# Optimization experiments

Hardware: AMD Instinct MI355X
Metric: run time of the kernel (lower is better)

Reference implementation:

```python
import jax, jax.numpy as jnp
import numpy as np

B, N, D, H, R, K = 64, 197, 768, 3072, 16, 1


def setup_inputs() -> dict:
    key = jax.random.key(0)
    ks = jax.random.split(key, 9)
    s1 = 1.0 / np.sqrt(D)
    s2 = 1.0 / np.sqrt(H)
    return {
        "x": jax.random.normal(ks[0], (B, N, D), dtype=jnp.float32),
        "W1": jax.random.normal(ks[1], (H, D), dtype=jnp.float32) * s1,
        "b1": jax.random.normal(ks[2], (H,), dtype=jnp.float32) * s1,
        "A1": jax.random.normal(ks[3], (K, R, D), dtype=jnp.float32) * s1,
        "B1": jax.random.normal(ks[4], (K, H, R), dtype=jnp.float32) * 0.01,
        "W2": jax.random.normal(ks[5], (D, H), dtype=jnp.float32) * s2,
        "b2": jax.random.normal(ks[6], (D,), dtype=jnp.float32) * s2,
        "A2": jax.random.normal(ks[7], (K, R, H), dtype=jnp.float32) * s2,
        "B2": jax.random.normal(ks[8], (K, D, R), dtype=jnp.float32) * 0.01,
    }


def _lora(x, A, Bm):
    # result of torch: (B @ (A @ x^T.unsqueeze(1))).sum(1).transpose(1,2)
    # A: [K, r, d_in], Bm: [K, d_out, r], x: [b, n, d_in] -> [b, n, d_out]
    t = jnp.einsum('krd,bnd->bknr', A, x)          # low-rank projection
    return jnp.einsum('kor,bknr->bno', Bm, t)      # expand + sum over K


def reference(x, W1, b1, A1, B1, W2, b2, A2, B2):
    # fc1 (Linear + LoRA correction)
    h = jnp.einsum('bnd,hd->bnh', x, W1) + b1 + _lora(x, A1, B1)
    # exact (erf-based) GELU, matching torch nn.GELU default
    h = jax.nn.gelu(h, approximate=False)
    # dropout p=0 and norm=Identity by default -> no-ops
    out = jnp.einsum('bnh,dh->bnd', h, W2) + b2 + _lora(h, A2, B2)
    return out
```

## Files before the change

### kernel.cpp

```cpp
#include <hip/hip_runtime.h>
#include <math.h>

#define M_ROWS 12608
#define D_DIM  768
#define H_DIM  3072

typedef __bf16 bf16_t;
typedef __bf16 bf16x8 __attribute__((ext_vector_type(8)));
typedef float  f32x4  __attribute__((ext_vector_type(4)));

__device__ __forceinline__ void gl2lds16(const bf16_t* g, bf16_t* l) {
  __builtin_amdgcn_global_load_lds(
      (__attribute__((address_space(1))) void*)g,
      (__attribute__((address_space(3))) void*)l,
      16, 0, 0);
}

__device__ __forceinline__ float gelu_fast(float v) {
  float v2 = v * v;
  float z = v * fmaf(0.044715f, v2, 1.0f);
  float e = __expf(-1.5957691216057308f * z);
  return v * __builtin_amdgcn_rcpf(1.0f + e);
}

__global__ void cast_f32_bf16_kernel(const float* __restrict__ in,
                                     bf16_t* __restrict__ out, long n) {
  long i = ((long)blockIdx.x * 256 + threadIdx.x) * 4;
  if (i + 3 < n) {
    float4 v = *(const float4*)(in + i);
    out[i + 0] = (bf16_t)v.x; out[i + 1] = (bf16_t)v.y;
    out[i + 2] = (bf16_t)v.z; out[i + 3] = (bf16_t)v.w;
  } else {
    for (; i < n; ++i) out[i] = (bf16_t)in[i];
  }
}

__global__ void fold_lora_kernel(const float* __restrict__ W,
                                 const float* __restrict__ A,
                                 const float* __restrict__ Bm,
                                 bf16_t* __restrict__ Weff,
                                 int OUT, int IN) {
  long idx = (long)blockIdx.x * 256 + threadIdx.x;
  if (idx >= (long)OUT * IN) return;
  int o = (int)(idx / IN);
  int i = (int)(idx - (long)o * IN);
  float s = W[idx];
#pragma unroll
  for (int r = 0; r < 16; ++r)
    s += Bm[o * 16 + r] * A[r * IN + i];
  Weff[idx] = (bf16_t)s;
}

template <bool GELU, typename OutT, int SMEM_BYTES>
__global__ __launch_bounds__(256, 3) void gemm_kernel(
    const bf16_t* __restrict__ Amat, const bf16_t* __restrict__ Bmat,
    const float* __restrict__ bias, OutT* __restrict__ Cmat,
    int Mrows, int Ncols, int Kd, int nColT, int nRowT) {
  __shared__ char smem[SMEM_BYTES];
  bf16_t* lds = (bf16_t*)smem;
  float* sT = (float*)smem;

  const int xcd = blockIdx.x & 7, tswz = blockIdx.x >> 3;
  const int colb = tswz % nColT, rband = tswz / nColT;
  const int rowb = rband * 8 + xcd;
  if (rowb >= nRowT) return;
  const int row0 = rowb * 128, col0 = colb * 128;

  const int tid = threadIdx.x, lane = tid & 63, wave = tid >> 6;
  const int wm = wave & 1, wn = wave >> 1;

  const bf16_t* gA[2]; const bf16_t* gB[2];
  int stA[2], stB[2];
#pragma unroll
  for (int q = 0; q < 2; ++q) {
    int c = tid + q * 256;
    int r = c >> 2;
    int kcg = (c & 3) ^ ((r >> 1) & 3);
    int ra = row0 + r; if (ra > Mrows - 1) ra = Mrows - 1;
    gA[q] = Amat + (size_t)ra * Kd + kcg * 8;
    stA[q] = (q * 256 + wave * 64) * 8;
    gB[q] = Bmat + (size_t)(col0 + r) * Kd + kcg * 8;
    stB[q] = 4096 + (q * 256 + wave * 64) * 8;
  }

  const int rl = lane & 15, kc = lane >> 4;
  int aoffs[4], boffs[4];
#pragma unroll
  for (int i = 0; i < 4; ++i) {
    int ra = wm * 64 + i * 16 + rl;
    int rb = wn * 64 + i * 16 + rl;
    aoffs[i] = ra * 32 + ((kc ^ ((ra >> 1) & 3)) * 8);
    boffs[i] = 4096 + rb * 32 + ((kc ^ ((rb >> 1) & 3)) * 8);
  }

  auto issue = [&](int par) {
    bf16_t* bb = lds + par * 8192;
    gl2lds16(gA[0], bb + stA[0]); gl2lds16(gA[1], bb + stA[1]);
    gl2lds16(gB[0], bb + stB[0] - 4096 + 4096); gl2lds16(gB[1], bb + stB[1] - 4096 + 4096);
    gA[0] += 32; gA[1] += 32; gB[0] += 32; gB[1] += 32;
  };

  f32x4 acc[4][4] = {};
  const int iters = Kd / 32;

  issue(0);
  for (int it = 0; it < iters; ++it) {
    __syncthreads();
    if (it + 1 < iters) issue((it + 1) & 1);
    const bf16_t* buf = lds + (it & 1) * 8192;
    bf16x8 af[4], bfr[4];
#pragma unroll
    for (int i = 0; i < 4; ++i) af[i] = *(const bf16x8*)(buf + aoffs[i]);
#pragma unroll
    for (int i = 0; i < 4; ++i) bfr[i] = *(const bf16x8*)(buf + boffs[i]);
#pragma unroll
    for (int mi = 0; mi < 4; ++mi)
#pragma unroll
      for (int ni = 0; ni < 4; ++ni)
        acc[mi][ni] = __builtin_amdgcn_mfma_f32_16x16x32_bf16(
            af[mi], bfr[ni], acc[mi][ni], 0, 0, 0);
  }

  const int crow = (lane >> 4) * 4, ccol = lane & 15;
  if constexpr (GELU) {
    __syncthreads();
#pragma unroll
    for (int p = 0; p < 2; ++p) {
#pragma unroll
      for (int s = 0; s < 2; ++s) {
        int mi = 2 * p + s;
#pragma unroll
        for (int ni = 0; ni < 4; ++ni)
#pragma unroll
          for (int r = 0; r < 4; ++r)
            sT[(wm * 32 + s * 16 + crow + r) * 132 + wn * 64 + ni * 16 + ccol] =
                acc[mi][ni][r];
      }
      __syncthreads();
      const int erow = tid >> 2, eseg = tid & 3;
      const int grow = row0 + (erow >> 5) * 64 + (2 * p + ((erow >> 4) & 1)) * 16 + (erow & 15);
      if (grow < Mrows) {
        const float* src = sT + erow * 132 + eseg * 32;
        const float* bsrc = bias + col0 + eseg * 32;
        bf16_t ov[32];
#pragma unroll
        for (int i = 0; i < 32; ++i)
          ov[i] = (bf16_t)gelu_fast(src[i] + bsrc[i]);
        bf16_t* dst = (bf16_t*)Cmat + (size_t)grow * Ncols + col0 + eseg * 32;
#pragma unroll
        for (int k = 0; k < 4; ++k)
          *(bf16x8*)(dst + k * 8) = *(bf16x8*)(ov + k * 8);
      }
      __syncthreads();
    }
  } else {
#pragma unroll
    for (int ni = 0; ni < 4; ++ni) {
      const int gc = col0 + wn * 64 + ni * 16 + ccol;
      const float bv = bias[gc];
#pragma unroll
      for (int mi = 0; mi < 4; ++mi) {
        const int gr = row0 + wm * 64 + mi * 16 + crow;
#pragma unroll
        for (int r = 0; r < 4; ++r) {
          const int row = gr + r;
          if (row < Mrows)
            Cmat[(size_t)row * Ncols + gc] = acc[mi][ni][r] + bv;
        }
      }
    }
  }
}

extern "C" void kernel_launch(void* const* d_in, const int* in_sizes, int n_in,
                              void* d_out, int out_size, void* d_ws, size_t ws_size,
                              hipStream_t stream) {
  const float* x  = (const float*)d_in[0];
  const float* W1 = (const float*)d_in[1];
  const float* b1 = (const float*)d_in[2];
  const float* A1 = (const float*)d_in[3];
  const float* B1 = (const float*)d_in[4];
  const float* W2 = (const float*)d_in[5];
  const float* b2 = (const float*)d_in[6];
  const float* A2 = (const float*)d_in[7];
  const float* B2 = (const float*)d_in[8];
  float* out = (float*)d_out;

  char* ws = (char*)d_ws;
  bf16_t* xb    = (bf16_t*)ws;
  bf16_t* W1eff = (bf16_t*)(ws + 19366144);
  bf16_t* W2eff = (bf16_t*)(ws + 19366144 + 4718592);
  bf16_t* hbuf  = (bf16_t*)(ws + 19366144 + 2 * 4718592);

  const long nx = (long)M_ROWS * D_DIM;
  cast_f32_bf16_kernel<<<(int)((nx / 4 + 255) / 256), 256, 0, stream>>>(x, xb, nx);

  const int foldBlocks = (H_DIM * D_DIM + 255) / 256;
  fold_lora_kernel<<<foldBlocks, 256, 0, stream>>>(W1, A1, B1, W1eff, H_DIM, D_DIM);
  fold_lora_kernel<<<foldBlocks, 256, 0, stream>>>(W2, A2, B2, W2eff, D_DIM, H_DIM);

  gemm_kernel<true, bf16_t, 34048><<<2496, 256, 0, stream>>>(
      xb, W1eff, b1, hbuf, M_ROWS, H_DIM, D_DIM, 24, 99);
  gemm_kernel<false, float, 32768><<<624, 256, 0, stream>>>(
      hbuf, W2eff, b2, out, M_ROWS, D_DIM, H_DIM, 6, 99);
}
```

Measured before the change: 314.4 us.

## Stage GEMM tiles through registers with BK=64 and remap block-to-XCD scheduling

Both GEMMs previously loaded tiles straight into double-buffered LDS with global_load_lds. They now prefetch the next K-slab into registers during the MFMA work and store it to a single LDS buffer between two barriers. The K tile grows from 32 to 64, with an 8-way XOR swizzle matching the wider rows, so there are half as many loop iterations and barriers. Block-index decoding is hardcoded per GEMM so that blocks on the same XCD share row or column tiles, and the second GEMM's grid shrinks to 600 blocks. The aim is better L2 reuse and fewer synchronisation points. The cost is more registers and a serialising store-sync step, which could hurt occupancy and overlap.

```diff
diff --git a/kernel.cpp b/kernel.cpp
--- a/kernel.cpp
+++ b/kernel.cpp
@@ -8,13 +8,6 @@
 typedef __bf16 bf16_t;
 typedef __bf16 bf16x8 __attribute__((ext_vector_type(8)));
 typedef float  f32x4  __attribute__((ext_vector_type(4)));
-
-__device__ __forceinline__ void gl2lds16(const bf16_t* g, bf16_t* l) {
-  __builtin_amdgcn_global_load_lds(
-      (__attribute__((address_space(1))) void*)g,
-      (__attribute__((address_space(3))) void*)l,
-      16, 0, 0);
-}
 
 __device__ __forceinline__ float gelu_fast(float v) {
   float v2 = v * v;
@@ -51,36 +44,42 @@
   Weff[idx] = (bf16_t)s;
 }
 
-template <bool GELU, typename OutT, int SMEM_BYTES>
+template <bool GELU, typename OutT, int SCHED, int SMEM_BYTES>
 __global__ __launch_bounds__(256, 3) void gemm_kernel(
     const bf16_t* __restrict__ Amat, const bf16_t* __restrict__ Bmat,
     const float* __restrict__ bias, OutT* __restrict__ Cmat,
-    int Mrows, int Ncols, int Kd, int nColT, int nRowT) {
+    int Mrows, int Ncols, int Kd) {
   __shared__ char smem[SMEM_BYTES];
   bf16_t* lds = (bf16_t*)smem;
   float* sT = (float*)smem;
 
-  const int xcd = blockIdx.x & 7, tswz = blockIdx.x >> 3;
-  const int colb = tswz % nColT, rband = tswz / nColT;
-  const int rowb = rband * 8 + xcd;
-  if (rowb >= nRowT) return;
+  int rowb, colb;
+  const int xcd = blockIdx.x & 7, t = blockIdx.x >> 3;
+  if (SCHED == 1) {
+    colb = t / 13;
+    rowb = (t % 13) * 8 + xcd;
+    if (rowb >= 99) return;
+  } else {
+    rowb = (t / 3) * 4 + (xcd & 3);
+    if (rowb >= 99) return;
+    colb = (xcd >> 2) * 3 + (t % 3);
+  }
   const int row0 = rowb * 128, col0 = colb * 128;
 
   const int tid = threadIdx.x, lane = tid & 63, wave = tid >> 6;
   const int wm = wave & 1, wn = wave >> 1;
 
-  const bf16_t* gA[2]; const bf16_t* gB[2];
-  int stA[2], stB[2];
-#pragma unroll
-  for (int q = 0; q < 2; ++q) {
+  const bf16_t* gA[4]; const bf16_t* gB[4];
+  int offA[4], offB[4];
+#pragma unroll
+  for (int q = 0; q < 4; ++q) {
     int c = tid + q * 256;
-    int r = c >> 2;
-    int kcg = (c & 3) ^ ((r >> 1) & 3);
+    int r = c >> 3, kkg = c & 7;
     int ra = row0 + r; if (ra > Mrows - 1) ra = Mrows - 1;
-    gA[q] = Amat + (size_t)ra * Kd + kcg * 8;
-    stA[q] = (q * 256 + wave * 64) * 8;
-    gB[q] = Bmat + (size_t)(col0 + r) * Kd + kcg * 8;
-    stB[q] = 4096 + (q * 256 + wave * 64) * 8;
+    gA[q] = Amat + (size_t)ra * Kd + kkg * 8;
+    offA[q] = r * 64 + (kkg ^ (r & 7)) * 8;
+    gB[q] = Bmat + (size_t)(col0 + r) * Kd + kkg * 8;
+    offB[q] = 8192 + r * 64 + (kkg ^ (r & 7)) * 8;
   }
 
   const int rl = lane & 15, kc = lane >> 4;
@@ -89,36 +88,58 @@
   for (int i = 0; i < 4; ++i) {
     int ra = wm * 64 + i * 16 + rl;
     int rb = wn * 64 + i * 16 + rl;
-    aoffs[i] = ra * 32 + ((kc ^ ((ra >> 1) & 3)) * 8);
-    boffs[i] = 4096 + rb * 32 + ((kc ^ ((rb >> 1) & 3)) * 8);
-  }
-
-  auto issue = [&](int par) {
-    bf16_t* bb = lds + par * 8192;
-    gl2lds16(gA[0], bb + stA[0]); gl2lds16(gA[1], bb + stA[1]);
-    gl2lds16(gB[0], bb + stB[0] - 4096 + 4096); gl2lds16(gB[1], bb + stB[1] - 4096 + 4096);
-    gA[0] += 32; gA[1] += 32; gB[0] += 32; gB[1] += 32;
-  };
+    aoffs[i] = ra * 64 + ((kc ^ (ra & 7)) * 8);
+    boffs[i] = 8192 + rb * 64 + ((kc ^ (rb & 7)) * 8);
+  }
 
   f32x4 acc[4][4] = {};
-  const int iters = Kd / 32;
-
-  issue(0);
+  f32x4 pA[4], pB[4];
+  const int iters = Kd / 64;
+
+#pragma unroll
+  for (int q = 0; q < 4; ++q) {
+    pA[q] = *(const f32x4*)gA[q]; pB[q] = *(const f32x4*)gB[q];
+    gA[q] += 64; gB[q] += 64;
+  }
+#pragma unroll
+  for (int q = 0; q < 4; ++q) {
+    *(f32x4*)(lds + offA[q]) = pA[q];
+    *(f32x4*)(lds + offB[q]) = pB[q];
+  }
+  __syncthreads();
+
   for (int it = 0; it < iters; ++it) {
-    __syncthreads();
-    if (it + 1 < iters) issue((it + 1) & 1);
-    const bf16_t* buf = lds + (it & 1) * 8192;
-    bf16x8 af[4], bfr[4];
-#pragma unroll
-    for (int i = 0; i < 4; ++i) af[i] = *(const bf16x8*)(buf + aoffs[i]);
-#pragma unroll
-    for (int i = 0; i < 4; ++i) bfr[i] = *(const bf16x8*)(buf + boffs[i]);
-#pragma unroll
-    for (int mi = 0; mi < 4; ++mi)
-#pragma unroll
-      for (int ni = 0; ni < 4; ++ni)
-        acc[mi][ni] = __builtin_amdgcn_mfma_f32_16x16x32_bf16(
-            af[mi], bfr[ni], acc[mi][ni], 0, 0, 0);
+    const bool more = (it + 1 < iters);
+    if (more) {
+#pragma unroll
+      for (int q = 0; q < 4; ++q) {
+        pA[q] = *(const f32x4*)gA[q]; pB[q] = *(const f32x4*)gB[q];
+        gA[q] += 64; gB[q] += 64;
+      }
+    }
+#pragma unroll
+    for (int ks = 0; ks < 2; ++ks) {
+      bf16x8 af[4], bfr[4];
+#pragma unroll
+      for (int i = 0; i < 4; ++i) af[i] = *(const bf16x8*)(lds + (aoffs[i] ^ (ks * 32)));
+#pragma unroll
+      for (int i = 0; i < 4; ++i) bfr[i] = *(const bf16x8*)(lds + (boffs[i] ^ (ks * 32)));
+#pragma unroll
+      for (int mi = 0; mi < 4; ++mi)
+#pragma unroll
+        for (int ni = 0; ni < 4; ++ni)
+          acc[mi][ni] = __builtin_amdgcn_mfma_f32_16x16x32_bf16(
+              af[mi], bfr[ni], acc[mi][ni], 0, 0, 0);
+    }
+    if (more) {
+      __syncthreads();
+#pragma unroll
+      for (int q = 0; q < 4; ++q) {
+        *(f32x4*)(lds + offA[q]) = pA[q];
+        *(f32x4*)(lds + offB[q]) = pB[q];
+      }
+      __syncthreads();
+    }
   }
 
   const int crow = (lane >> 4) * 4, ccol = lane & 15;
@@ -199,8 +220,8 @@
   fold_lora_kernel<<<foldBlocks, 256, 0, stream>>>(W1, A1, B1, W1eff, H_DIM, D_DIM);
   fold_lora_kernel<<<foldBlocks, 256, 0, stream>>>(W2, A2, B2, W2eff, D_DIM, H_DIM);
 
-  gemm_kernel<true, bf16_t, 34048><<<2496, 256, 0, stream>>>(
-      xb, W1eff, b1, hbuf, M_ROWS, H_DIM, D_DIM, 24, 99);
-  gemm_kernel<false, float, 32768><<<624, 256, 0, stream>>>(
-      hbuf, W2eff, b2, out, M_ROWS, D_DIM, H_DIM, 6, 99);
-}
+  gemm_kernel<true, bf16_t, 1, 33792><<<2496, 256, 0, stream>>>(
+      xb, W1eff, b1, hbuf, M_ROWS, H_DIM, D_DIM);
+  gemm_kernel<false, float, 2, 32768><<<600, 256, 0, stream>>>(
+      hbuf, W2eff, b2, out, M_ROWS, D_DIM, H_DIM);
+}
```

New measurement: 293.7 us. 1.07x faster.
